# Kernel tuning notes

Hardware: AMD Instinct MI355X
Metric: run time of the kernel (lower is better)

The kernel has to match this reference:

```python
import jax, jax.numpy as jnp
import numpy as np

VOCAB = 50257
EMBED = 256
HIDDEN = 128
NUM_CLASSES = 2
BATCH = 128
SEQ = 1024


def setup_inputs() -> dict:
    key = jax.random.key(0)
    ks = jax.random.split(key, 8)
    x = jax.random.randint(ks[0], (BATCH, SEQ), 0, VOCAB, dtype=jnp.int32).astype(jnp.int64)
    emb = jax.random.normal(ks[1], (VOCAB, EMBED), dtype=jnp.float32)
    emb = emb.at[0].set(0.0)  # padding_idx=0 row is zeros
    s = 1.0 / np.sqrt(HIDDEN)  # torch LSTM/Linear init scale
    W_ih = jax.random.uniform(ks[2], (4 * HIDDEN, EMBED), minval=-s, maxval=s, dtype=jnp.float32)
    W_hh = jax.random.uniform(ks[3], (4 * HIDDEN, HIDDEN), minval=-s, maxval=s, dtype=jnp.float32)
    b_ih = jax.random.uniform(ks[4], (4 * HIDDEN,), minval=-s, maxval=s, dtype=jnp.float32)
    b_hh = jax.random.uniform(ks[5], (4 * HIDDEN,), minval=-s, maxval=s, dtype=jnp.float32)
    W_fc = jax.random.uniform(ks[6], (NUM_CLASSES, HIDDEN), minval=-s, maxval=s, dtype=jnp.float32)
    b_fc = jax.random.uniform(ks[7], (NUM_CLASSES,), minval=-s, maxval=s, dtype=jnp.float32)
    return {"x": x, "emb": emb, "W_ih": W_ih, "W_hh": W_hh,
            "b_ih": b_ih, "b_hh": b_hh, "W_fc": W_fc, "b_fc": b_fc}


def reference(x, emb, W_ih, W_hh, b_ih, b_hh, W_fc, b_fc):
    # Embedding lookup: [B, T, E]
    embedded = emb[x]
    # Precompute input-to-hidden gate projections for all timesteps: [B, T, 4H]
    xg = jnp.einsum('bte,ge->btg', embedded, W_ih) + (b_ih + b_hh)
    B = x.shape[0]
    h0 = jnp.zeros((B, HIDDEN), dtype=emb.dtype)
    c0 = jnp.zeros((B, HIDDEN), dtype=emb.dtype)

    def step(carry, xt):
        h, c = carry
        gates = xt + h @ W_hh.T  # [B, 4H]
        i, f, g, o = jnp.split(gates, 4, axis=-1)  # torch gate order: i, f, g, o
        i = jax.nn.sigmoid(i)
        f = jax.nn.sigmoid(f)
        g = jnp.tanh(g)
        o = jax.nn.sigmoid(o)
        c = f * c + i * g
        h = o * jnp.tanh(c)
        return (h, c), None

    (h_T, c_T), _ = jax.lax.scan(step, (h0, c0), jnp.swapaxes(xg, 0, 1))
    # dropout is identity at inference; final linear head
    return h_T @ W_fc.T + b_fc
```

## Files before the change

### kernel.cpp

```cpp
#include <hip/hip_runtime.h>
#include <hip/hip_bf16.h>

#define VOCAB 50257
#define EMBED 256
#define HIDDEN 128
#define G4 512
#define BATCH 128
#define SEQ 1024

typedef float f32x4 __attribute__((ext_vector_type(4)));
typedef unsigned int u32x4 __attribute__((ext_vector_type(4)));

__device__ __forceinline__ float dpp_xor1(float x) {
    return __int_as_float(__builtin_amdgcn_update_dpp(
        0, __float_as_int(x), 0xB1 , 0xF, 0xF, true));
}
__device__ __forceinline__ float dpp_xor2(float x) {
    return __int_as_float(__builtin_amdgcn_update_dpp(
        0, __float_as_int(x), 0x4E , 0xF, 0xF, true));
}

__device__ __forceinline__ unsigned int bfbits(float f) {
    __hip_bfloat16 b = __float2bfloat16(f);
    return (unsigned int)*reinterpret_cast<unsigned short*>(&b);
}
__device__ __forceinline__ unsigned int pack2(float lo, float hi) {
    return bfbits(lo) | (bfbits(hi) << 16);
}
__device__ __forceinline__ float dot2bf(unsigned int a, unsigned int b, float c) {
    float d;
    asm("v_dot2_f32_bf16 %0, %1, %2, %3" : "=v"(d) : "v"(a), "v"(b), "v"(c));
    return d;
}

#define K1_BM 128
#define K1_BN 64
#define K1_BK 32

__global__ __launch_bounds__(256)
void table_gemm(const float* __restrict__ emb, const float* __restrict__ Wih,
                const float* __restrict__ bih, const float* __restrict__ bhh,
                float* __restrict__ table) {
    __shared__ __align__(16) float As[K1_BK][K1_BM + 4];
    __shared__ __align__(16) float Bs[K1_BK][K1_BN + 4];

    const int nTiles = G4 / K1_BN;
    const int mt = blockIdx.x / nTiles;
    const int nt = blockIdx.x % nTiles;
    const int m0 = mt * K1_BM, n0 = nt * K1_BN;
    const int tid  = threadIdx.x;
    const int tm   = tid & 15;
    const int tn   = tid >> 4;
    const int lrow = tid >> 3;
    const int lk   = (tid & 7) << 2;

    float acc[8][4];
#pragma unroll
    for (int i = 0; i < 8; ++i)
#pragma unroll
        for (int j = 0; j < 4; ++j) acc[i][j] = 0.f;

    for (int k0 = 0; k0 < EMBED; k0 += K1_BK) {
        __syncthreads();
#pragma unroll
        for (int p = 0; p < 4; ++p) {
            int m  = m0 + p * 32 + lrow;
            int ms = m < VOCAB ? m : VOCAB - 1;
            f32x4 a = *(const f32x4*)(emb + (size_t)ms * EMBED + k0 + lk);
            As[lk + 0][p * 32 + lrow] = a[0];
            As[lk + 1][p * 32 + lrow] = a[1];
            As[lk + 2][p * 32 + lrow] = a[2];
            As[lk + 3][p * 32 + lrow] = a[3];
        }
#pragma unroll
        for (int p = 0; p < 2; ++p) {
            int n = n0 + p * 32 + lrow;
            f32x4 b = *(const f32x4*)(Wih + (size_t)n * EMBED + k0 + lk);
            Bs[lk + 0][p * 32 + lrow] = b[0];
            Bs[lk + 1][p * 32 + lrow] = b[1];
            Bs[lk + 2][p * 32 + lrow] = b[2];
            Bs[lk + 3][p * 32 + lrow] = b[3];
        }
        __syncthreads();
#pragma unroll
        for (int k = 0; k < K1_BK; ++k) {
            f32x4 b4   = *(const f32x4*)&Bs[k][tn * 4];
            f32x4 a4lo = *(const f32x4*)&As[k][tm * 8];
            f32x4 a4hi = *(const f32x4*)&As[k][tm * 8 + 4];
#pragma unroll
            for (int i = 0; i < 4; ++i)
#pragma unroll
                for (int j = 0; j < 4; ++j) {
                    acc[i][j]     += a4lo[i] * b4[j];
                    acc[i + 4][j] += a4hi[i] * b4[j];
                }
        }
    }

    const int nbase = n0 + tn * 4;
    float bias0 = bih[nbase + 0] + bhh[nbase + 0];
    float bias1 = bih[nbase + 1] + bhh[nbase + 1];
    float bias2 = bih[nbase + 2] + bhh[nbase + 2];
    float bias3 = bih[nbase + 3] + bhh[nbase + 3];
#pragma unroll
    for (int i = 0; i < 8; ++i) {
        int m = m0 + tm * 8 + i;
        if (m < VOCAB) {
            f32x4 o;
            o[0] = acc[i][0] + bias0;
            o[1] = acc[i][1] + bias1;
            o[2] = acc[i][2] + bias2;
            o[3] = acc[i][3] + bias3;
            *(f32x4*)(table + (size_t)m * G4 + nbase) = o;
        }
    }
}

__global__ __launch_bounds__(512, 2)
void lstm_seq(const int* __restrict__ x, const float* __restrict__ table,
              const float* __restrict__ Whh,
              const float* __restrict__ Wfc, const float* __restrict__ bfc,
              float* __restrict__ out) {
    __shared__ __align__(16) unsigned short hbf[2][HIDDEN];
    __shared__ __align__(16) float hf[HIDDEN];
    __shared__ int toks[SEQ];

    const int b   = blockIdx.x;
    const int tid = threadIdx.x;
    const int j   = tid & 3;
    const int Q   = tid >> 2;

    for (int t = tid; t < SEQ; t += 512) toks[t] = x[b * SEQ + t];

    unsigned int wv[4][4][4];
#pragma unroll
    for (int m = 0; m < 4; ++m) {
        const float* wrow = Whh + (size_t)(m * HIDDEN + Q) * HIDDEN + 32 * j;
#pragma unroll
        for (int s = 0; s < 4; ++s) {
            const int cc = (s ^ j) & 3;
#pragma unroll
            for (int d = 0; d < 4; ++d)
                wv[m][s][d] = pack2(wrow[8 * cc + 2 * d], wrow[8 * cc + 2 * d + 1]);
        }
    }

    if (tid < HIDDEN) hbf[0][tid] = 0;
    float c = 0.f;
    const int lane_off = j * HIDDEN + Q;
    __syncthreads();

    float xg_cur = table[(size_t)toks[0] * G4 + lane_off];
    float xg_nxt = table[(size_t)toks[1] * G4 + lane_off];

    float h = 0.f;
    for (int t = 0; t < SEQ; ++t) {
        int   tk2   = toks[(t + 2) & (SEQ - 1)];
        float xg_n2 = table[(size_t)tk2 * G4 + lane_off];

        const char* hb = (const char*)hbf[t & 1] + 64 * j;
        u32x4 hc[4];
#pragma unroll
        for (int s = 0; s < 4; ++s)
            hc[s] = *(const u32x4*)(hb + 16 * ((s ^ j) & 3));

        float a0 = 0.f, a1 = 0.f, a2 = 0.f, a3 = 0.f;
#pragma unroll
        for (int s = 0; s < 4; ++s)
#pragma unroll
            for (int d = 0; d < 4; ++d) {
                a0 = dot2bf(wv[0][s][d], hc[s][d], a0);
                a1 = dot2bf(wv[1][s][d], hc[s][d], a1);
                a2 = dot2bf(wv[2][s][d], hc[s][d], a2);
                a3 = dot2bf(wv[3][s][d], hc[s][d], a3);
            }
        float p0 = a0 + ((j == 0) ? xg_cur : 0.f);
        float p1 = a1 + ((j == 1) ? xg_cur : 0.f);
        float p2 = a2 + ((j == 2) ? xg_cur : 0.f);
        float p3 = a3 + ((j == 3) ? xg_cur : 0.f);

        float u0 = p0 + dpp_xor1(p0);
        float u1 = p1 + dpp_xor1(p1);
        float u2 = p2 + dpp_xor1(p2);
        float u3 = p3 + dpp_xor1(p3);
        float v0 = (j & 1) ? u2 : u0;
        float v1 = (j & 1) ? u3 : u1;
        float w0 = v0 + dpp_xor2(v0);
        float w1 = v1 + dpp_xor2(v1);
        float o0 = dpp_xor1(w0);
        float o1 = dpp_xor1(w1);
        float gi = (j & 1) ? o0 : w0;
        float gf = (j & 1) ? o1 : w1;
        float gg = (j & 1) ? w0 : o0;
        float go = (j & 1) ? w1 : o1;

        float si = __builtin_amdgcn_rcpf(1.f + __expf(-gi));
        float sf = __builtin_amdgcn_rcpf(1.f + __expf(-gf));
        float so = __builtin_amdgcn_rcpf(1.f + __expf(-go));
        float eg = __expf(2.f * gg);
        float tg = 1.f - 2.f * __builtin_amdgcn_rcpf(eg + 1.f);
        c = sf * c + si * tg;
        float ec = __expf(2.f * c);
        float tc = 1.f - 2.f * __builtin_amdgcn_rcpf(ec + 1.f);
        h = so * tc;

        const int nxt = (t + 1) & 1;
        if (j == 0)
            hbf[nxt][Q] = (unsigned short)bfbits(h);
        __syncthreads();

        xg_cur = xg_nxt;
        xg_nxt = xg_n2;
    }

    if (j == 0) hf[Q] = h;
    __syncthreads();
    if (tid < 2) {
        const f32x4* wf = (const f32x4*)(Wfc + tid * HIDDEN);
        const f32x4* h4 = (const f32x4*)hf;
        f32x4 s = {0.f, 0.f, 0.f, 0.f};
#pragma unroll
        for (int k = 0; k < 32; ++k) s += wf[k] * h4[k];
        out[b * 2 + tid] = bfc[tid] + ((s[0] + s[1]) + (s[2] + s[3]));
    }
}

extern "C" void kernel_launch(void* const* d_in, const int* in_sizes, int n_in,
                              void* d_out, int out_size, void* d_ws, size_t ws_size,
                              hipStream_t stream) {
    (void)in_sizes; (void)n_in; (void)out_size; (void)ws_size;
    const int*   x   = (const int*)d_in[0];
    const float* emb = (const float*)d_in[1];
    const float* Wih = (const float*)d_in[2];
    const float* Whh = (const float*)d_in[3];
    const float* bih = (const float*)d_in[4];
    const float* bhh = (const float*)d_in[5];
    const float* Wfc = (const float*)d_in[6];
    const float* bfc = (const float*)d_in[7];
    float* out   = (float*)d_out;
    float* table = (float*)d_ws;

    const int mTiles = (VOCAB + K1_BM - 1) / K1_BM;
    const int nTiles = G4 / K1_BN;
    table_gemm<<<dim3(mTiles * nTiles), 256, 0, stream>>>(emb, Wih, bih, bhh, table);
    lstm_seq<<<dim3(BATCH), 512, 0, stream>>>(x, table, Whh, Wfc, bfc, out);
}
```

Before: 860.5 us.

## Halve LSTM block threads by giving each lane two hidden units

The recurrent kernel now runs 256 threads per batch row instead of 512, with each 4-lane group computing two hidden units (8 gate rows held as bf16 weights in registers). The cross-lane gate reduction is reworked with DPP broadcasts, and the two new h values are packed with a single cvt_pk_bf16 store. The aim is to cut per-step barrier cost and wave count for the serial 1024-step recurrence, at the cost of doubling per-thread dot-product work and register pressure (128 weight registers).

```diff
diff --git a/kernel.cpp b/kernel.cpp
--- a/kernel.cpp
+++ b/kernel.cpp
@@ -9,6 +9,7 @@
 #define SEQ 1024
 
 typedef float f32x4 __attribute__((ext_vector_type(4)));
+typedef float f32x2 __attribute__((ext_vector_type(2)));
 typedef unsigned int u32x4 __attribute__((ext_vector_type(4)));
 
 __device__ __forceinline__ float dpp_xor1(float x) {
@@ -18,6 +19,22 @@
 __device__ __forceinline__ float dpp_xor2(float x) {
     return __int_as_float(__builtin_amdgcn_update_dpp(
         0, __float_as_int(x), 0x4E , 0xF, 0xF, true));
+}
+__device__ __forceinline__ float dpp_bc0(float x) {
+    return __int_as_float(__builtin_amdgcn_update_dpp(
+        0, __float_as_int(x), 0x00, 0xF, 0xF, true));
+}
+__device__ __forceinline__ float dpp_bc1(float x) {
+    return __int_as_float(__builtin_amdgcn_update_dpp(
+        0, __float_as_int(x), 0x55, 0xF, 0xF, true));
+}
+__device__ __forceinline__ float dpp_bc2(float x) {
+    return __int_as_float(__builtin_amdgcn_update_dpp(
+        0, __float_as_int(x), 0xAA, 0xF, 0xF, true));
+}
+__device__ __forceinline__ float dpp_bc3(float x) {
+    return __int_as_float(__builtin_amdgcn_update_dpp(
+        0, __float_as_int(x), 0xFF, 0xF, 0xF, true));
 }
 
 __device__ __forceinline__ unsigned int bfbits(float f) {
@@ -26,6 +43,11 @@
 }
 __device__ __forceinline__ unsigned int pack2(float lo, float hi) {
     return bfbits(lo) | (bfbits(hi) << 16);
+}
+__device__ __forceinline__ unsigned int cvt_pk_bf16(float lo, float hi) {
+    unsigned int r;
+    asm("v_cvt_pk_bf16_f32 %0, %1, %2" : "=v"(r) : "v"(lo), "v"(hi));
+    return r;
 }
 __device__ __forceinline__ float dot2bf(unsigned int a, unsigned int b, float c) {
     float d;
@@ -116,7 +138,7 @@
     }
 }
 
-__global__ __launch_bounds__(512, 2)
+__global__ __launch_bounds__(256, 1)
 void lstm_seq(const int* __restrict__ x, const float* __restrict__ table,
               const float* __restrict__ Whh,
               const float* __restrict__ Wfc, const float* __restrict__ bfc,
@@ -130,12 +152,13 @@
     const int j   = tid & 3;
     const int Q   = tid >> 2;
 
-    for (int t = tid; t < SEQ; t += 512) toks[t] = x[b * SEQ + t];
-
-    unsigned int wv[4][4][4];
-#pragma unroll
-    for (int m = 0; m < 4; ++m) {
-        const float* wrow = Whh + (size_t)(m * HIDDEN + Q) * HIDDEN + 32 * j;
+    for (int t = tid; t < SEQ; t += 256) toks[t] = x[b * SEQ + t];
+
+    unsigned int wv[8][4][4];
+#pragma unroll
+    for (int m = 0; m < 8; ++m) {
+        const float* wrow =
+            Whh + (size_t)((m & 3) * HIDDEN + 2 * Q + (m >> 2)) * HIDDEN + 32 * j;
 #pragma unroll
         for (int s = 0; s < 4; ++s) {
             const int cc = (s ^ j) & 3;
@@ -146,17 +169,17 @@
     }
 
     if (tid < HIDDEN) hbf[0][tid] = 0;
-    float c = 0.f;
-    const int lane_off = j * HIDDEN + Q;
+    float cA = 0.f, cB = 0.f;
+    const int xgoff = j * HIDDEN + 2 * Q;
     __syncthreads();
 
-    float xg_cur = table[(size_t)toks[0] * G4 + lane_off];
-    float xg_nxt = table[(size_t)toks[1] * G4 + lane_off];
-
-    float h = 0.f;
+    f32x2 xg_cur = *(const f32x2*)(table + (size_t)toks[0] * G4 + xgoff);
+    f32x2 xg_nxt = *(const f32x2*)(table + (size_t)toks[1] * G4 + xgoff);
+
+    float hA = 0.f, hB = 0.f;
     for (int t = 0; t < SEQ; ++t) {
         int   tk2   = toks[(t + 2) & (SEQ - 1)];
-        float xg_n2 = table[(size_t)tk2 * G4 + lane_off];
+        f32x2 xg_n2 = *(const f32x2*)(table + (size_t)tk2 * G4 + xgoff);
 
         const char* hb = (const char*)hbf[t & 1] + 64 * j;
         u32x4 hc[4];
@@ -164,56 +187,74 @@
         for (int s = 0; s < 4; ++s)
             hc[s] = *(const u32x4*)(hb + 16 * ((s ^ j) & 3));
 
-        float a0 = 0.f, a1 = 0.f, a2 = 0.f, a3 = 0.f;
+        float p[8];
+#pragma unroll
+        for (int m = 0; m < 8; ++m) p[m] = 0.f;
 #pragma unroll
         for (int s = 0; s < 4; ++s)
 #pragma unroll
-            for (int d = 0; d < 4; ++d) {
-                a0 = dot2bf(wv[0][s][d], hc[s][d], a0);
-                a1 = dot2bf(wv[1][s][d], hc[s][d], a1);
-                a2 = dot2bf(wv[2][s][d], hc[s][d], a2);
-                a3 = dot2bf(wv[3][s][d], hc[s][d], a3);
-            }
-        float p0 = a0 + ((j == 0) ? xg_cur : 0.f);
-        float p1 = a1 + ((j == 1) ? xg_cur : 0.f);
-        float p2 = a2 + ((j == 2) ? xg_cur : 0.f);
-        float p3 = a3 + ((j == 3) ? xg_cur : 0.f);
-
-        float u0 = p0 + dpp_xor1(p0);
-        float u1 = p1 + dpp_xor1(p1);
-        float u2 = p2 + dpp_xor1(p2);
-        float u3 = p3 + dpp_xor1(p3);
-        float v0 = (j & 1) ? u2 : u0;
-        float v1 = (j & 1) ? u3 : u1;
-        float w0 = v0 + dpp_xor2(v0);
-        float w1 = v1 + dpp_xor2(v1);
-        float o0 = dpp_xor1(w0);
-        float o1 = dpp_xor1(w1);
-        float gi = (j & 1) ? o0 : w0;
-        float gf = (j & 1) ? o1 : w1;
-        float gg = (j & 1) ? w0 : o0;
-        float go = (j & 1) ? w1 : o1;
-
-        float si = __builtin_amdgcn_rcpf(1.f + __expf(-gi));
-        float sf = __builtin_amdgcn_rcpf(1.f + __expf(-gf));
-        float so = __builtin_amdgcn_rcpf(1.f + __expf(-go));
-        float eg = __expf(2.f * gg);
-        float tg = 1.f - 2.f * __builtin_amdgcn_rcpf(eg + 1.f);
-        c = sf * c + si * tg;
-        float ec = __expf(2.f * c);
-        float tc = 1.f - 2.f * __builtin_amdgcn_rcpf(ec + 1.f);
-        h = so * tc;
+            for (int d = 0; d < 4; ++d)
+#pragma unroll
+                for (int m = 0; m < 8; ++m)
+                    p[m] = dot2bf(wv[m][s][d], hc[s][d], p[m]);
+
+#pragma unroll
+        for (int m = 0; m < 4; ++m) {
+            p[m]     += (j == m) ? xg_cur[0] : 0.f;
+            p[m + 4] += (j == m) ? xg_cur[1] : 0.f;
+        }
+
+        float u[8];
+#pragma unroll
+        for (int m = 0; m < 8; ++m) u[m] = p[m] + dpp_xor1(p[m]);
+        const bool bit0 = (j & 1);
+        float a0 = bit0 ? u[1] : u[0];
+        float a1 = bit0 ? u[3] : u[2];
+        float a2 = bit0 ? u[5] : u[4];
+        float a3 = bit0 ? u[7] : u[6];
+        float A0 = a0 + dpp_xor2(a0);
+        float A1 = a1 + dpp_xor2(a1);
+        float A2 = a2 + dpp_xor2(a2);
+        float A3 = a3 + dpp_xor2(a3);
+        const bool bit1 = (j & 2);
+        float preA = bit1 ? A1 : A0;
+        float preB = bit1 ? A3 : A2;
+
+        float giA = dpp_bc0(preA), gfA = dpp_bc1(preA);
+        float ggA = dpp_bc2(preA), goA = dpp_bc3(preA);
+        float giB = dpp_bc0(preB), gfB = dpp_bc1(preB);
+        float ggB = dpp_bc2(preB), goB = dpp_bc3(preB);
+
+        float siA = __builtin_amdgcn_rcpf(1.f + __expf(-giA));
+        float sfA = __builtin_amdgcn_rcpf(1.f + __expf(-gfA));
+        float soA = __builtin_amdgcn_rcpf(1.f + __expf(-goA));
+        float egA = __expf(2.f * ggA);
+        float tgA = 1.f - 2.f * __builtin_amdgcn_rcpf(egA + 1.f);
+        cA = sfA * cA + siA * tgA;
+        float ecA = __expf(2.f * cA);
+        float tcA = 1.f - 2.f * __builtin_amdgcn_rcpf(ecA + 1.f);
+        hA = soA * tcA;
+
+        float siB = __builtin_amdgcn_rcpf(1.f + __expf(-giB));
+        float sfB = __builtin_amdgcn_rcpf(1.f + __expf(-gfB));
+        float soB = __builtin_amdgcn_rcpf(1.f + __expf(-goB));
+        float egB = __expf(2.f * ggB);
+        float tgB = 1.f - 2.f * __builtin_amdgcn_rcpf(egB + 1.f);
+        cB = sfB * cB + siB * tgB;
+        float ecB = __expf(2.f * cB);
+        float tcB = 1.f - 2.f * __builtin_amdgcn_rcpf(ecB + 1.f);
+        hB = soB * tcB;
 
         const int nxt = (t + 1) & 1;
         if (j == 0)
-            hbf[nxt][Q] = (unsigned short)bfbits(h);
+            *(unsigned int*)((char*)hbf[nxt] + 4 * Q) = cvt_pk_bf16(hA, hB);
         __syncthreads();
 
         xg_cur = xg_nxt;
         xg_nxt = xg_n2;
     }
 
-    if (j == 0) hf[Q] = h;
+    if (j == 0) { hf[2 * Q] = hA; hf[2 * Q + 1] = hB; }
     __syncthreads();
     if (tid < 2) {
         const f32x4* wf = (const f32x4*)(Wfc + tid * HIDDEN);
@@ -243,5 +284,5 @@
     const int mTiles = (VOCAB + K1_BM - 1) / K1_BM;
     const int nTiles = G4 / K1_BN;
     table_gemm<<<dim3(mTiles * nTiles), 256, 0, stream>>>(emb, Wih, bih, bhh, table);
-    lstm_seq<<<dim3(BATCH), 512, 0, stream>>>(x, table, Whh, Wfc, bfc, out);
-}
+    lstm_seq<<<dim3(BATCH), 256, 0, stream>>>(x, table, Whh, Wfc, bfc, out);
+}
```

After: 859.8 us. Within noise of the previous version (-0.1%).
